# Performance work log

Hardware: AMD Instinct MI355X
Metric: run time of the kernel (lower is better)

## Reference

```python
import jax, jax.numpy as jnp
import numpy as np

T = 4096      # sentence length
V = 50257     # vocab size
E = 1024      # embedding dim
H = 512       # hidden per direction (hidden_dim // 2)
NT = 32       # tagset size


def setup_inputs() -> dict:
    key = jax.random.key(0)
    ks = jax.random.split(key, 12)
    s = 0.02
    return {
        "sentence": jax.random.randint(ks[0], (T,), 0, V, dtype=jnp.int32),
        "emb": jax.random.normal(ks[1], (V, E), jnp.float32) * s,
        "W_ih_f": jax.random.normal(ks[2], (3 * H, E), jnp.float32) * s,
        "W_hh_f": jax.random.normal(ks[3], (3 * H, H), jnp.float32) * s,
        "b_ih_f": jax.random.normal(ks[4], (3 * H,), jnp.float32) * s,
        "b_hh_f": jax.random.normal(ks[5], (3 * H,), jnp.float32) * s,
        "W_ih_b": jax.random.normal(ks[6], (3 * H, E), jnp.float32) * s,
        "W_hh_b": jax.random.normal(ks[7], (3 * H, H), jnp.float32) * s,
        "b_ih_b": jax.random.normal(ks[8], (3 * H,), jnp.float32) * s,
        "b_hh_b": jax.random.normal(ks[9], (3 * H,), jnp.float32) * s,
        "W_out": jax.random.normal(ks[10], (NT, E), jnp.float32) * s,
    }


def _gru_dir(x, W_ih, W_hh, b_ih, b_hh):
    """Run a single-direction GRU over x [T, E] -> hidden states [T, H].
    PyTorch GRU gate math: r,z,n order; h' = (1-z)*n + z*h; h0 = 0."""
    gi = x @ W_ih.T + b_ih  # [T, 3H] input projections, one big GEMM

    def step(h, gi_t):
        gh = h @ W_hh.T + b_hh            # [3H]
        ir, iz, inn = jnp.split(gi_t, 3)
        hr, hz, hn = jnp.split(gh, 3)
        r = jax.nn.sigmoid(ir + hr)
        z = jax.nn.sigmoid(iz + hz)
        n = jnp.tanh(inn + r * hn)
        h_new = (1.0 - z) * n + z * h
        return h_new, h_new

    h0 = jnp.zeros((W_hh.shape[1],), x.dtype)
    _, hs = jax.lax.scan(step, h0, gi)
    return hs  # [T, H]


def reference(sentence, emb, W_ih_f, W_hh_f, b_ih_f, b_hh_f,
              W_ih_b, W_hh_b, b_ih_b, b_hh_b, W_out):
    x = emb[sentence]  # [T, E] embedding lookup
    h_fwd = _gru_dir(x, W_ih_f, W_hh_f, b_ih_f, b_hh_f)            # [T, H]
    h_bwd = _gru_dir(x[::-1], W_ih_b, W_hh_b, b_ih_b, b_hh_b)[::-1]  # [T, H]
    h = jnp.concatenate([h_fwd, h_bwd], axis=-1)  # [T, 2H]
    return h @ W_out.T  # [T, NT] tag scores (no bias)
```

## Files before the change

kernel.cpp:

```cpp
#include <hip/hip_runtime.h>

#define T_LEN 4096
#define E_DIM 1024
#define H_DIM 512
#define NT_DIM 32
#define NG 3072

typedef __attribute__((ext_vector_type(8))) short bf16x8;
typedef __attribute__((ext_vector_type(4))) float f32x4;
typedef __attribute__((ext_vector_type(4))) unsigned int u32x4;
typedef unsigned long long ull;

__device__ inline unsigned short f2bf(float f) {
    unsigned int u = __float_as_uint(f);
    unsigned int r = (u + 0x7fffu + ((u >> 16) & 1u)) >> 16;
    return (unsigned short)r;
}
__device__ inline float bf2f(unsigned short u) {
    return __uint_as_float(((unsigned int)u) << 16);
}
__device__ inline ull packhs(float v, unsigned tag) {
    return (ull)__float_as_uint(v) | ((ull)tag << 32);
}

__global__ void embed_cast(const int* __restrict__ sent, const float* __restrict__ emb,
                           unsigned short* __restrict__ xb) {
    int t = blockIdx.x;
    int row = sent[t];
    const float4* src = (const float4*)(emb + (size_t)row * E_DIM);
    ushort4* dst = (ushort4*)(xb + (size_t)t * E_DIM);
    float4 v = src[threadIdx.x];
    ushort4 o;
    o.x = f2bf(v.x); o.y = f2bf(v.y); o.z = f2bf(v.z); o.w = f2bf(v.w);
    dst[threadIdx.x] = o;
}

__global__ void wcast(const float* __restrict__ wf, const float* __restrict__ wb_,
                      unsigned short* __restrict__ w) {
    int r = blockIdx.x;
    const float* src = (r < 1536) ? (wf + (size_t)r * E_DIM) : (wb_ + (size_t)(r - 1536) * E_DIM);
    const float4* s4 = (const float4*)src;
    ushort4* dst = (ushort4*)(w + (size_t)r * E_DIM);
    float4 v = s4[threadIdx.x];
    ushort4 o;
    o.x = f2bf(v.x); o.y = f2bf(v.y); o.z = f2bf(v.z); o.w = f2bf(v.w);
    dst[threadIdx.x] = o;
}

#define LDST 40
__global__ __launch_bounds__(256) void gi_gemm(const unsigned short* __restrict__ xb,
                                               const unsigned short* __restrict__ wb,
                                               const float* __restrict__ bihf,
                                               const float* __restrict__ bihb,
                                               unsigned short* __restrict__ gi) {
    __shared__ __align__(16) unsigned short As[64 * LDST];
    __shared__ __align__(16) unsigned short Bs[64 * LDST];
    int tile_m = (blockIdx.x % 64) * 64;
    int tile_n = (blockIdx.x / 64) * 64;
    int tid = threadIdx.x;
    int lane = tid & 63, wv = tid >> 6;
    int quad = lane >> 4, r15 = lane & 15;
    int srow = tid >> 2, sseg = tid & 3;

    f32x4 acc[4] = {};
    for (int kb = 0; kb < E_DIM; kb += 32) {
        uint4 a = *(const uint4*)(xb + (size_t)(tile_m + srow) * E_DIM + kb + sseg * 8);
        uint4 b = *(const uint4*)(wb + (size_t)(tile_n + srow) * E_DIM + kb + sseg * 8);
        *(uint4*)&As[srow * LDST + sseg * 8] = a;
        *(uint4*)&Bs[srow * LDST + sseg * 8] = b;
        __syncthreads();
        bf16x8 af = *(bf16x8*)&As[(wv * 16 + r15) * LDST + quad * 8];
#pragma unroll
        for (int nt = 0; nt < 4; nt++) {
            bf16x8 bf = *(bf16x8*)&Bs[(nt * 16 + r15) * LDST + quad * 8];
            acc[nt] = __builtin_amdgcn_mfma_f32_16x16x32_bf16(af, bf, acc[nt], 0, 0, 0);
        }
        __syncthreads();
    }
#pragma unroll
    for (int nt = 0; nt < 4; nt++) {
        int gn = tile_n + nt * 16 + r15;
        float bias = (gn < 1536) ? bihf[gn] : bihb[gn - 1536];
#pragma unroll
        for (int rg = 0; rg < 4; rg++) {
            int gm = tile_m + wv * 16 + quad * 4 + rg;
            gi[(size_t)gm * NG + gn] = f2bf(acc[nt][rg] + bias);
        }
    }
}

__global__ __launch_bounds__(512, 2) void gru_rec(
    const float* __restrict__ whhf, const float* __restrict__ bhhf,
    const float* __restrict__ whhb, const float* __restrict__ bhhb,
    const unsigned short* __restrict__ gi, ull* __restrict__ hxf, ull* __restrict__ hxb) {
    int dir = blockIdx.x >> 4;
    int g   = blockIdx.x & 15;
    const float* whh = dir ? whhb : whhf;
    const float* bhh = dir ? bhhb : bhhf;
    ull* hx = dir ? hxb : hxf;

    int tid = threadIdx.x;
    int w = tid >> 6;
    int l = tid & 63;
    int q = l & 15;
    int o = l >> 4;
    int c = g * 32 + w * 4 + o;

    float4 wr[8], wz[8], wn[8];
#pragma unroll
    for (int j = 0; j < 8; j++) {
        wr[j] = *(const float4*)(whh + (size_t)c * H_DIM + q * 32 + j * 4);
        wz[j] = *(const float4*)(whh + (size_t)(c + 512) * H_DIM + q * 32 + j * 4);
        wn[j] = *(const float4*)(whh + (size_t)(c + 1024) * H_DIM + q * 32 + j * 4);
    }
    bool owner = (q == 0);
    float bias_r = 0.f, bias_z = 0.f, bias_n = 0.f, h_own = 0.f;
    if (owner) { bias_r = bhh[c]; bias_z = bhh[c + 512]; bias_n = bhh[c + 1024]; }

    __shared__ float hsh[576];
    for (int i = tid; i < 576; i += 512) hsh[i] = 0.f;
    __syncthreads();

    for (int s = 0; s < T_LEN; s++) {
        int row = dir ? (T_LEN - 1 - s) : s;
        float gir = 0.f, giz = 0.f, gin = 0.f;
        if (owner) {
            const unsigned short* gp = gi + (size_t)row * NG + dir * 1536 + c;
            gir = bf2f(gp[0]); giz = bf2f(gp[512]); gin = bf2f(gp[1024]);
        }

        float hv[8];
        if (w == 0 && s > 0) {
            int prow = dir ? (T_LEN - s) : (s - 1);
            ull addr = (ull)(hx + (size_t)prow * H_DIM + 8 * l);
            unsigned et = (unsigned)s;
            u32x4 d0, d1, d2, d3;
            for (;;) {
                asm volatile("global_load_dwordx4 %0, %1, off sc0 sc1" : "=v"(d0) : "v"(addr));
                asm volatile("global_load_dwordx4 %0, %1, off offset:16 sc0 sc1" : "=v"(d1) : "v"(addr));
                asm volatile("global_load_dwordx4 %0, %1, off offset:32 sc0 sc1" : "=v"(d2) : "v"(addr));
                asm volatile("global_load_dwordx4 %0, %1, off offset:48 sc0 sc1" : "=v"(d3) : "v"(addr));
                asm volatile("s_waitcnt vmcnt(0)" ::: "memory");
                __builtin_amdgcn_sched_barrier(0);
                bool ok = (d0.y == et) & (d0.w == et) & (d1.y == et) & (d1.w == et)
                        & (d2.y == et) & (d2.w == et) & (d3.y == et) & (d3.w == et);
                if (ok) break;
            }
            hv[0] = __uint_as_float(d0.x); hv[1] = __uint_as_float(d0.z);
            hv[2] = __uint_as_float(d1.x); hv[3] = __uint_as_float(d1.z);
            hv[4] = __uint_as_float(d2.x); hv[5] = __uint_as_float(d2.z);
            hv[6] = __uint_as_float(d3.x); hv[7] = __uint_as_float(d3.z);
        }
        __syncthreads();
        if (w == 0 && s > 0) {
            int base = 8 * l + 4 * (l >> 2);
            float4 va = { hv[0], hv[1], hv[2], hv[3] };
            float4 vb = { hv[4], hv[5], hv[6], hv[7] };
            *(float4*)&hsh[base]     = va;
            *(float4*)&hsh[base + 4] = vb;
        }
        __syncthreads();

        float pr = 0.f, pz = 0.f, pn = 0.f;
        const float* hb = &hsh[36 * q];
#pragma unroll
        for (int j = 0; j < 8; j++) {
            float4 h4 = *(const float4*)(hb + 4 * j);
            pr += wr[j].x * h4.x + wr[j].y * h4.y + wr[j].z * h4.z + wr[j].w * h4.w;
            pz += wz[j].x * h4.x + wz[j].y * h4.y + wz[j].z * h4.z + wz[j].w * h4.w;
            pn += wn[j].x * h4.x + wn[j].y * h4.y + wn[j].z * h4.z + wn[j].w * h4.w;
        }
        pr += __shfl_xor(pr, 1); pz += __shfl_xor(pz, 1); pn += __shfl_xor(pn, 1);
        pr += __shfl_xor(pr, 2); pz += __shfl_xor(pz, 2); pn += __shfl_xor(pn, 2);
        pr += __shfl_xor(pr, 4); pz += __shfl_xor(pz, 4); pn += __shfl_xor(pn, 4);
        pr += __shfl_xor(pr, 8); pz += __shfl_xor(pz, 8); pn += __shfl_xor(pn, 8);

        if (owner) {
            float rr = 1.f / (1.f + __expf(-(gir + pr + bias_r)));
            float zz = 1.f / (1.f + __expf(-(giz + pz + bias_z)));
            float a = gin + rr * (pn + bias_n);
            a = fminf(20.f, fmaxf(-20.f, a));
            float e = __expf(-2.f * a);
            float nn = (1.f - e) / (1.f + e);
            float hnew = (1.f - zz) * nn + zz * h_own;
            h_own = hnew;
            __hip_atomic_store(hx + (size_t)row * H_DIM + c, packhs(hnew, (unsigned)(s + 1)),
                               __ATOMIC_RELAXED, __HIP_MEMORY_SCOPE_AGENT);
        }
    }
}

__global__ __launch_bounds__(256) void out_gemm(const ull* __restrict__ hxf,
                                                const ull* __restrict__ hxb,
                                                const float* __restrict__ wout,
                                                float* __restrict__ out) {
    __shared__ __align__(16) float ls[8][1028];
    int t0 = blockIdx.x * 8;
    int tid = threadIdx.x;
#pragma unroll
    for (int i = 0; i < 8; i++) {
        int col = tid * 4;
        const ull* src = (col < 512) ? (hxf + (size_t)(t0 + i) * H_DIM + col)
                                     : (hxb + (size_t)(t0 + i) * H_DIM + (col - 512));
        ull s0 = src[0], s1 = src[1], s2 = src[2], s3 = src[3];
        ls[i][col + 0] = __uint_as_float((unsigned)s0);
        ls[i][col + 1] = __uint_as_float((unsigned)s1);
        ls[i][col + 2] = __uint_as_float((unsigned)s2);
        ls[i][col + 3] = __uint_as_float((unsigned)s3);
    }
    __syncthreads();
    int r8 = tid >> 5, gg = tid & 31;
    const float4* wp = (const float4*)(wout + (size_t)gg * 1024);
    float sum = 0.f;
#pragma unroll 8
    for (int j = 0; j < 256; j++) {
        float4 w = wp[j];
        float4 h = *(const float4*)&ls[r8][j * 4];
        sum += w.x * h.x + w.y * h.y + w.z * h.z + w.w * h.w;
    }
    out[(size_t)(t0 + r8) * NT_DIM + gg] = sum;
}

extern "C" void kernel_launch(void* const* d_in, const int* in_sizes, int n_in,
                              void* d_out, int out_size, void* d_ws, size_t ws_size,
                              hipStream_t stream) {
    const int*   sent = (const int*)d_in[0];
    const float* emb  = (const float*)d_in[1];
    const float* wihf = (const float*)d_in[2];
    const float* whhf = (const float*)d_in[3];
    const float* bihf = (const float*)d_in[4];
    const float* bhhf = (const float*)d_in[5];
    const float* wihb = (const float*)d_in[6];
    const float* whhb = (const float*)d_in[7];
    const float* bihb = (const float*)d_in[8];
    const float* bhhb = (const float*)d_in[9];
    const float* wout = (const float*)d_in[10];

    char* ws = (char*)d_ws;
    unsigned short* gi  = (unsigned short*)(ws);
    unsigned short* xb  = (unsigned short*)(ws + 25165824);
    unsigned short* wb  = (unsigned short*)(ws + 33554432);
    ull*            hxf = (ull*)(ws + 39845888);
    ull*            hxb = (ull*)(ws + 56623104);
    float*          out = (float*)d_out;

    embed_cast<<<T_LEN, 256, 0, stream>>>(sent, emb, xb);
    wcast<<<NG, 256, 0, stream>>>(wihf, wihb, wb);
    gi_gemm<<<64 * 48, 256, 0, stream>>>(xb, wb, bihf, bihb, gi);
    gru_rec<<<32, 512, 0, stream>>>(whhf, bhhf, whhb, bhhb, gi, hxf, hxb);
    out_gemm<<<T_LEN / 8, 256, 0, stream>>>(hxf, hxb, wout, out);
}
```

Measured before the change: 7.291 ms.

## Spread GRU recurrence over more workgroups and add per-XCD fast ring buffer for h exchange

The recurrent kernel now launches 512 blocks of 256 threads and keeps only those whose index mod 8 is 0 or 1, so each direction's 64 worker blocks (8 hidden columns each) are likely placed on the same XCD. Each step's h is also written to a small 64-row ring buffer, which readers poll with device-coherent-lite loads (sc0 only), falling back to the fully coherent slow path after a bounded number of tries. The aim is to cut the cross-XCD synchronisation latency of the per-step h exchange and to spread the matvec over more CUs. An init kernel zeroes the hx and ring buffers first. The change relies on round-robin XCD placement of blocks, and the ring buffer reuses workspace regions (xb/wb) that are already consumed by then.

```diff
diff --git a/kernel.cpp b/kernel.cpp
--- a/kernel.cpp
+++ b/kernel.cpp
@@ -89,37 +89,55 @@
     }
 }
 
-__global__ __launch_bounds__(512, 2) void gru_rec(
+__global__ __launch_bounds__(256) void init_hx(ull* __restrict__ hxf, ull* __restrict__ hxb,
+                                               ull* __restrict__ ff, ull* __restrict__ fb) {
+    size_t stride = (size_t)gridDim.x * 256;
+    size_t i = (size_t)blockIdx.x * 256 + threadIdx.x;
+    for (size_t j = i; j < 2097152; j += stride) { hxf[j] = 0; hxb[j] = 0; }
+    if (i < 32768) { ff[i] = 0; fb[i] = 0; }
+}
+
+__global__ __launch_bounds__(256, 2) void gru_rec(
     const float* __restrict__ whhf, const float* __restrict__ bhhf,
     const float* __restrict__ whhb, const float* __restrict__ bhhb,
-    const unsigned short* __restrict__ gi, ull* __restrict__ hxf, ull* __restrict__ hxb) {
-    int dir = blockIdx.x >> 4;
-    int g   = blockIdx.x & 15;
+    const unsigned short* __restrict__ gi,
+    ull* __restrict__ hxf, ull* __restrict__ hxb,
+    ull* __restrict__ fastf, ull* __restrict__ fastb) {
+    int x8 = blockIdx.x & 7;
+    if (x8 > 1) return;
+    int dir = x8;
+    int g = blockIdx.x >> 3;
     const float* whh = dir ? whhb : whhf;
     const float* bhh = dir ? bhhb : bhhf;
-    ull* hx = dir ? hxb : hxf;
-
-    int tid = threadIdx.x;
-    int w = tid >> 6;
-    int l = tid & 63;
-    int q = l & 15;
-    int o = l >> 4;
-    int c = g * 32 + w * 4 + o;
-
-    float4 wr[8], wz[8], wn[8];
-#pragma unroll
-    for (int j = 0; j < 8; j++) {
-        wr[j] = *(const float4*)(whh + (size_t)c * H_DIM + q * 32 + j * 4);
-        wz[j] = *(const float4*)(whh + (size_t)(c + 512) * H_DIM + q * 32 + j * 4);
-        wn[j] = *(const float4*)(whh + (size_t)(c + 1024) * H_DIM + q * 32 + j * 4);
-    }
-    bool owner = (q == 0);
+    ull* hx   = dir ? hxb   : hxf;
+    ull* fast = dir ? fastb : fastf;
+
+    int t = threadIdx.x;
+    int w = t >> 6;
+    int l = t & 63;
+    int kq = l & 31;
+    int half = l >> 5;
+    int c = g * 8 + w * 2 + half;
+    bool owner = (kq == 0);
+
+    float4 wr[4], wz[4], wn[4];
+    {
+        const float* pw = whh + (size_t)c * H_DIM + kq * 16;
+#pragma unroll
+        for (int j = 0; j < 4; j++) {
+            wr[j] = *(const float4*)(pw + j * 4);
+            wz[j] = *(const float4*)(pw + 512 * H_DIM + j * 4);
+            wn[j] = *(const float4*)(pw + 1024 * H_DIM + j * 4);
+        }
+    }
     float bias_r = 0.f, bias_z = 0.f, bias_n = 0.f, h_own = 0.f;
     if (owner) { bias_r = bhh[c]; bias_z = bhh[c + 512]; bias_n = bhh[c + 1024]; }
 
-    __shared__ float hsh[576];
-    for (int i = tid; i < 576; i += 512) hsh[i] = 0.f;
+    __shared__ __align__(16) float hsh[640];
+    for (int i = t; i < 640; i += 256) hsh[i] = 0.f;
     __syncthreads();
+
+    bool fast_on = true;
 
     for (int s = 0; s < T_LEN; s++) {
         int row = dir ? (T_LEN - 1 - s) : s;
@@ -132,19 +150,38 @@
         float hv[8];
         if (w == 0 && s > 0) {
             int prow = dir ? (T_LEN - s) : (s - 1);
-            ull addr = (ull)(hx + (size_t)prow * H_DIM + 8 * l);
             unsigned et = (unsigned)s;
+            ull fa = (ull)(fast + ((size_t)(prow & 63) * H_DIM + 8 * l));
+            ull sa = (ull)(hx + ((size_t)prow * H_DIM + 8 * l));
             u32x4 d0, d1, d2, d3;
-            for (;;) {
-                asm volatile("global_load_dwordx4 %0, %1, off sc0 sc1" : "=v"(d0) : "v"(addr));
-                asm volatile("global_load_dwordx4 %0, %1, off offset:16 sc0 sc1" : "=v"(d1) : "v"(addr));
-                asm volatile("global_load_dwordx4 %0, %1, off offset:32 sc0 sc1" : "=v"(d2) : "v"(addr));
-                asm volatile("global_load_dwordx4 %0, %1, off offset:48 sc0 sc1" : "=v"(d3) : "v"(addr));
-                asm volatile("s_waitcnt vmcnt(0)" ::: "memory");
-                __builtin_amdgcn_sched_barrier(0);
-                bool ok = (d0.y == et) & (d0.w == et) & (d1.y == et) & (d1.w == et)
-                        & (d2.y == et) & (d2.w == et) & (d3.y == et) & (d3.w == et);
-                if (ok) break;
+            bool got = false;
+            if (fast_on) {
+                int tries = (s == 1) ? 4096 : 24;
+                for (int it = 0; it < tries; ++it) {
+                    asm volatile("global_load_dwordx4 %0, %1, off sc0" : "=v"(d0) : "v"(fa));
+                    asm volatile("global_load_dwordx4 %0, %1, off offset:16 sc0" : "=v"(d1) : "v"(fa));
+                    asm volatile("global_load_dwordx4 %0, %1, off offset:32 sc0" : "=v"(d2) : "v"(fa));
+                    asm volatile("global_load_dwordx4 %0, %1, off offset:48 sc0" : "=v"(d3) : "v"(fa));
+                    asm volatile("s_waitcnt vmcnt(0)" ::: "memory");
+                    __builtin_amdgcn_sched_barrier(0);
+                    bool ok = (d0.y == et) & (d0.w == et) & (d1.y == et) & (d1.w == et)
+                            & (d2.y == et) & (d2.w == et) & (d3.y == et) & (d3.w == et);
+                    if (__all(ok)) { got = true; break; }
+                }
+                if (!got) fast_on = false;
+            }
+            if (!got) {
+                for (;;) {
+                    asm volatile("global_load_dwordx4 %0, %1, off sc0 sc1" : "=v"(d0) : "v"(sa));
+                    asm volatile("global_load_dwordx4 %0, %1, off offset:16 sc0 sc1" : "=v"(d1) : "v"(sa));
+                    asm volatile("global_load_dwordx4 %0, %1, off offset:32 sc0 sc1" : "=v"(d2) : "v"(sa));
+                    asm volatile("global_load_dwordx4 %0, %1, off offset:48 sc0 sc1" : "=v"(d3) : "v"(sa));
+                    asm volatile("s_waitcnt vmcnt(0)" ::: "memory");
+                    __builtin_amdgcn_sched_barrier(0);
+                    bool ok = (d0.y == et) & (d0.w == et) & (d1.y == et) & (d1.w == et)
+                            & (d2.y == et) & (d2.w == et) & (d3.y == et) & (d3.w == et);
+                    if (__all(ok)) break;
+                }
             }
             hv[0] = __uint_as_float(d0.x); hv[1] = __uint_as_float(d0.z);
             hv[2] = __uint_as_float(d1.x); hv[3] = __uint_as_float(d1.z);
@@ -153,27 +190,35 @@
         }
         __syncthreads();
         if (w == 0 && s > 0) {
-            int base = 8 * l + 4 * (l >> 2);
-            float4 va = { hv[0], hv[1], hv[2], hv[3] };
-            float4 vb = { hv[4], hv[5], hv[6], hv[7] };
-            *(float4*)&hsh[base]     = va;
-            *(float4*)&hsh[base + 4] = vb;
+            int base = (l >> 1) * 20 + (l & 1) * 8;
+            *(float4*)&hsh[base]     = make_float4(hv[0], hv[1], hv[2], hv[3]);
+            *(float4*)&hsh[base + 4] = make_float4(hv[4], hv[5], hv[6], hv[7]);
         }
         __syncthreads();
 
-        float pr = 0.f, pz = 0.f, pn = 0.f;
-        const float* hb = &hsh[36 * q];
-#pragma unroll
-        for (int j = 0; j < 8; j++) {
-            float4 h4 = *(const float4*)(hb + 4 * j);
-            pr += wr[j].x * h4.x + wr[j].y * h4.y + wr[j].z * h4.z + wr[j].w * h4.w;
-            pz += wz[j].x * h4.x + wz[j].y * h4.y + wz[j].z * h4.z + wz[j].w * h4.w;
-            pn += wn[j].x * h4.x + wn[j].y * h4.y + wn[j].z * h4.z + wn[j].w * h4.w;
-        }
-        pr += __shfl_xor(pr, 1); pz += __shfl_xor(pz, 1); pn += __shfl_xor(pn, 1);
-        pr += __shfl_xor(pr, 2); pz += __shfl_xor(pz, 2); pn += __shfl_xor(pn, 2);
-        pr += __shfl_xor(pr, 4); pz += __shfl_xor(pz, 4); pn += __shfl_xor(pn, 4);
-        pr += __shfl_xor(pr, 8); pz += __shfl_xor(pz, 8); pn += __shfl_xor(pn, 8);
+        const float* hb = &hsh[kq * 20];
+        float4 h0 = *(const float4*)(hb);
+        float4 h1 = *(const float4*)(hb + 4);
+        float4 h2 = *(const float4*)(hb + 8);
+        float4 h3 = *(const float4*)(hb + 12);
+        float pr, pz, pn;
+        pr  = wr[0].x * h0.x + wr[0].y * h0.y + wr[0].z * h0.z + wr[0].w * h0.w
+            + wr[1].x * h1.x + wr[1].y * h1.y + wr[1].z * h1.z + wr[1].w * h1.w
+            + wr[2].x * h2.x + wr[2].y * h2.y + wr[2].z * h2.z + wr[2].w * h2.w
+            + wr[3].x * h3.x + wr[3].y * h3.y + wr[3].z * h3.z + wr[3].w * h3.w;
+        pz  = wz[0].x * h0.x + wz[0].y * h0.y + wz[0].z * h0.z + wz[0].w * h0.w
+            + wz[1].x * h1.x + wz[1].y * h1.y + wz[1].z * h1.z + wz[1].w * h1.w
+            + wz[2].x * h2.x + wz[2].y * h2.y + wz[2].z * h2.z + wz[2].w * h2.w
+            + wz[3].x * h3.x + wz[3].y * h3.y + wz[3].z * h3.z + wz[3].w * h3.w;
+        pn  = wn[0].x * h0.x + wn[0].y * h0.y + wn[0].z * h0.z + wn[0].w * h0.w
+            + wn[1].x * h1.x + wn[1].y * h1.y + wn[1].z * h1.z + wn[1].w * h1.w
+            + wn[2].x * h2.x + wn[2].y * h2.y + wn[2].z * h2.z + wn[2].w * h2.w
+            + wn[3].x * h3.x + wn[3].y * h3.y + wn[3].z * h3.z + wn[3].w * h3.w;
+        pr += __shfl_xor(pr, 1);  pz += __shfl_xor(pz, 1);  pn += __shfl_xor(pn, 1);
+        pr += __shfl_xor(pr, 2);  pz += __shfl_xor(pz, 2);  pn += __shfl_xor(pn, 2);
+        pr += __shfl_xor(pr, 4);  pz += __shfl_xor(pz, 4);  pn += __shfl_xor(pn, 4);
+        pr += __shfl_xor(pr, 8);  pz += __shfl_xor(pz, 8);  pn += __shfl_xor(pn, 8);
+        pr += __shfl_xor(pr, 16); pz += __shfl_xor(pz, 16); pn += __shfl_xor(pn, 16);
 
         if (owner) {
             float rr = 1.f / (1.f + __expf(-(gir + pr + bias_r)));
@@ -184,7 +229,10 @@
             float nn = (1.f - e) / (1.f + e);
             float hnew = (1.f - zz) * nn + zz * h_own;
             h_own = hnew;
-            __hip_atomic_store(hx + (size_t)row * H_DIM + c, packhs(hnew, (unsigned)(s + 1)),
+            ull pv = packhs(hnew, (unsigned)(s + 1));
+            ull faddr = (ull)(fast + ((size_t)(row & 63) * H_DIM + c));
+            asm volatile("global_store_dwordx2 %0, %1, off sc0" :: "v"(faddr), "v"(pv) : "memory");
+            __hip_atomic_store(hx + (size_t)row * H_DIM + c, pv,
                                __ATOMIC_RELAXED, __HIP_MEMORY_SCOPE_AGENT);
         }
     }
@@ -242,11 +290,14 @@
     unsigned short* wb  = (unsigned short*)(ws + 33554432);
     ull*            hxf = (ull*)(ws + 39845888);
     ull*            hxb = (ull*)(ws + 56623104);
+    ull*            fastf = (ull*)(ws + 25165824);
+    ull*            fastb = (ull*)(ws + 33554432);
     float*          out = (float*)d_out;
 
     embed_cast<<<T_LEN, 256, 0, stream>>>(sent, emb, xb);
     wcast<<<NG, 256, 0, stream>>>(wihf, wihb, wb);
     gi_gemm<<<64 * 48, 256, 0, stream>>>(xb, wb, bihf, bihb, gi);
-    gru_rec<<<32, 512, 0, stream>>>(whhf, bhhf, whhb, bhhb, gi, hxf, hxb);
+    init_hx<<<2048, 256, 0, stream>>>(hxf, hxb, fastf, fastb);
+    gru_rec<<<512, 256, 0, stream>>>(whhf, bhhf, whhb, bhhb, gi, hxf, hxb, fastf, fastb);
     out_gemm<<<T_LEN / 8, 256, 0, stream>>>(hxf, hxb, wout, out);
 }
```

Measured after the change: 7.421 ms. Within noise of the previous version (+1.8%).
